# Kernel tuning notes

Hardware: AMD Instinct MI355X
Metric: run time of the kernel (lower is better)

The kernel has to match this reference:

```python
import jax, jax.numpy as jnp
import numpy as np

N = 50000      # nodes
E = 1600000    # edges
IN_DIM = 128
HID = 32
OUT = 32
HEADS = 4
NEG_SLOPE = 0.2  # DGL GATConv default leaky_relu slope


def setup_inputs() -> dict:
    key = jax.random.key(0)
    ks = jax.random.split(key, 16)
    h = jax.random.normal(ks[0], (N, IN_DIM), dtype=jnp.float32)
    src = jax.random.randint(ks[1], (E,), 0, N, dtype=jnp.int32)
    dst = jax.random.randint(ks[2], (E,), 0, N, dtype=jnp.int32)
    s = 0.1
    # layer 1: in_dim -> (HEADS, HID)
    W1 = jax.random.normal(ks[3], (IN_DIM, HEADS * HID), dtype=jnp.float32) * s
    al1 = jax.random.normal(ks[4], (HEADS, HID), dtype=jnp.float32) * s
    ar1 = jax.random.normal(ks[5], (HEADS, HID), dtype=jnp.float32) * s
    b1 = jnp.zeros((HEADS * HID,), dtype=jnp.float32)
    # layer 2: HEADS*HID -> (HEADS, HID)
    W2 = jax.random.normal(ks[6], (HEADS * HID, HEADS * HID), dtype=jnp.float32) * s
    al2 = jax.random.normal(ks[7], (HEADS, HID), dtype=jnp.float32) * s
    ar2 = jax.random.normal(ks[8], (HEADS, HID), dtype=jnp.float32) * s
    b2 = jnp.zeros((HEADS * HID,), dtype=jnp.float32)
    # layer 3: HEADS*HID -> (HEADS, OUT)
    W3 = jax.random.normal(ks[9], (HEADS * HID, HEADS * OUT), dtype=jnp.float32) * s
    al3 = jax.random.normal(ks[10], (HEADS, OUT), dtype=jnp.float32) * s
    ar3 = jax.random.normal(ks[11], (HEADS, OUT), dtype=jnp.float32) * s
    b3 = jnp.zeros((HEADS * OUT,), dtype=jnp.float32)
    return {"h": h, "src": src, "dst": dst,
            "W1": W1, "al1": al1, "ar1": ar1, "b1": b1,
            "W2": W2, "al2": al2, "ar2": ar2, "b2": b2,
            "W3": W3, "al3": al3, "ar3": ar3, "b3": b3}


def gat_layer(h, W, al, ar, b, src, dst):
    """DGL-style GATConv. h:[N,F] -> [N,H,D]."""
    H, D = al.shape
    ft = (h @ W).reshape(-1, H, D)                      # [N,H,D]
    el = jnp.einsum('nhd,hd->nh', ft, al)               # [N,H]
    er = jnp.einsum('nhd,hd->nh', ft, ar)               # [N,H]
    e = jax.nn.leaky_relu(el[src] + er[dst], NEG_SLOPE)  # [E,H]
    # edge softmax grouped by destination node
    m = jax.ops.segment_max(e, dst, num_segments=N)     # [N,H]
    ex = jnp.exp(e - m[dst])
    z = jax.ops.segment_sum(ex, dst, num_segments=N)    # [N,H]
    a = ex / z[dst]                                     # [E,H]
    msg = ft[src] * a[:, :, None]                       # [E,H,D]
    rst = jax.ops.segment_sum(msg, dst, num_segments=N)  # [N,H,D]
    return rst + b.reshape(1, H, D)


def reference(h, src, dst, W1, al1, ar1, b1, W2, al2, ar2, b2, W3, al3, ar3, b3):
    x = gat_layer(h, W1, al1, ar1, b1, src, dst).reshape(N, -1)  # flatten(1)
    x = jax.nn.elu(x)  # dropout is identity at eval
    x = gat_layer(x, W2, al2, ar2, b2, src, dst).reshape(N, -1)
    x = jax.nn.elu(x)
    x = gat_layer(x, W3, al3, ar3, b3, src, dst).mean(axis=1)    # [N,OUT]
    return x
```

## Files before the change

### kernel.cpp

```cpp
#include <hip/hip_runtime.h>
#include <hip/hip_fp16.h>

#define NEG_SLOPE 0.2f
#define LOG2E 1.44269504088896340736f
#define C1   2048
#define BKT  196
#define BSTR 9216

typedef _Float16 half8 __attribute__((ext_vector_type(8)));

__device__ __forceinline__ unsigned int encf(float f) {
    unsigned int u = __float_as_uint(f);
    return (u & 0x80000000u) ? ~u : (u | 0x80000000u);
}
__device__ __forceinline__ float decf(unsigned int u) {
    return (u & 0x80000000u) ? __uint_as_float(u & 0x7fffffffu)
                             : __uint_as_float(~u);
}

__global__ __launch_bounds__(256) void gemm128(const float* __restrict__ X,
    const float* __restrict__ W, const float* __restrict__ al,
    const float* __restrict__ ar, __half* __restrict__ C16,
    float* __restrict__ el, float* __restrict__ er,
    unsigned int* __restrict__ maxbuf, int M)
{
    __shared__ float Xs[32][68];
    __shared__ float Ws[32][128];
    __shared__ unsigned int lmax[8];
    const int t    = threadIdx.x;
    const int row0 = blockIdx.x * 64;
    const int rg   = t >> 5;
    const int cg   = t & 31;
    float acc[8][4];
#pragma unroll
    for (int i = 0; i < 8; ++i) { acc[i][0]=0.f; acc[i][1]=0.f; acc[i][2]=0.f; acc[i][3]=0.f; }
    if (t < 8) lmax[t] = 0;

    for (int kc = 0; kc < 4; ++kc) {
        const int k0 = kc * 32;
        {
            const int lr = t >> 2;
            const int lk = (t & 3) * 8;
            int gr = row0 + lr; if (gr >= M) gr = M - 1;
            const float4* s4 = (const float4*)&X[(size_t)gr * 128 + k0 + lk];
            float4 a = s4[0], b = s4[1];
            Xs[lk+0][lr]=a.x; Xs[lk+1][lr]=a.y; Xs[lk+2][lr]=a.z; Xs[lk+3][lr]=a.w;
            Xs[lk+4][lr]=b.x; Xs[lk+5][lr]=b.y; Xs[lk+6][lr]=b.z; Xs[lk+7][lr]=b.w;
        }
        {
            const int lk = t >> 3;
            const int lc = (t & 7) * 16;
            const float4* s4 = (const float4*)&W[(size_t)(k0 + lk) * 128 + lc];
            float4* dd = (float4*)&Ws[lk][lc];
            dd[0]=s4[0]; dd[1]=s4[1]; dd[2]=s4[2]; dd[3]=s4[3];
        }
        __syncthreads();
#pragma unroll
        for (int k = 0; k < 32; ++k) {
            float4 wv = *(const float4*)&Ws[k][cg * 4];
            float4 x0 = *(const float4*)&Xs[k][rg * 8];
            float4 x1 = *(const float4*)&Xs[k][rg * 8 + 4];
            float xr[8] = {x0.x,x0.y,x0.z,x0.w,x1.x,x1.y,x1.z,x1.w};
#pragma unroll
            for (int i = 0; i < 8; ++i) {
                acc[i][0] += xr[i] * wv.x;
                acc[i][1] += xr[i] * wv.y;
                acc[i][2] += xr[i] * wv.z;
                acc[i][3] += xr[i] * wv.w;
            }
        }
        __syncthreads();
    }
#pragma unroll
    for (int i = 0; i < 8; ++i) {
        int gr = row0 + rg * 8 + i;
        if (gr < M) {
            __half2 h0 = __floats2half2_rn(acc[i][0], acc[i][1]);
            __half2 h1 = __floats2half2_rn(acc[i][2], acc[i][3]);
            uint2 pv;
            pv.x = __builtin_bit_cast(unsigned int, h0);
            pv.y = __builtin_bit_cast(unsigned int, h1);
            *(uint2*)&C16[(size_t)gr * 128 + cg * 4] = pv;
        }
    }
    {
        float4 alv = *(const float4*)&al[cg * 4];
        float4 arv = *(const float4*)&ar[cg * 4];
        alv.x *= LOG2E; alv.y *= LOG2E; alv.z *= LOG2E; alv.w *= LOG2E;
        arv.x *= LOG2E; arv.y *= LOG2E; arv.z *= LOG2E; arv.w *= LOG2E;
        float pl[8], pr[8];
#pragma unroll
        for (int i = 0; i < 8; ++i) {
            pl[i] = acc[i][0]*alv.x + acc[i][1]*alv.y + acc[i][2]*alv.z + acc[i][3]*alv.w;
            pr[i] = acc[i][0]*arv.x + acc[i][1]*arv.y + acc[i][2]*arv.z + acc[i][3]*arv.w;
        }
#pragma unroll
        for (int off = 1; off < 8; off <<= 1) {
#pragma unroll
            for (int i = 0; i < 8; ++i) {
                pl[i] += __shfl_xor(pl[i], off);
                pr[i] += __shfl_xor(pr[i], off);
            }
        }
        if ((cg & 7) == 0) {
            const int head = cg >> 3;
            float plm = pl[0], prm = pr[0];
#pragma unroll
            for (int i = 1; i < 8; ++i) { plm = fmaxf(plm, pl[i]); prm = fmaxf(prm, pr[i]); }
            atomicMax(&lmax[head], encf(plm));
            atomicMax(&lmax[4 + head], encf(prm));
#pragma unroll
            for (int i = 0; i < 8; ++i) {
                int gr = row0 + rg * 8 + i;
                if (gr < M) {
                    el[(size_t)gr * 4 + head] = pl[i];
                    er[(size_t)gr * 4 + head] = pr[i];
                }
            }
        }
        __syncthreads();
        if (t < 8) atomicMax(&maxbuf[t], lmax[t]);
    }
}

__global__ __launch_bounds__(256) void p1_bucket(const int* __restrict__ src,
    const int* __restrict__ dst, unsigned int* __restrict__ tmp,
    unsigned int* __restrict__ bcnt, int E_)
{
    __shared__ unsigned int hist[256];
    __shared__ unsigned int sc[256];
    __shared__ unsigned int ebase[256];
    __shared__ unsigned int gbase[256];
    __shared__ unsigned int buf[C1];
    const int t  = threadIdx.x;
    const int e0 = blockIdx.x * C1;
    hist[t] = 0;
    __syncthreads();
    int  s_[8], d_[8];
    bool v_[8];
#pragma unroll
    for (int k = 0; k < 2; ++k) {
        int idx = e0 + k * 1024 + t * 4;
        if (idx + 3 < E_) {
            int4 sv = *(const int4*)&src[idx];
            int4 dv = *(const int4*)&dst[idx];
            s_[k*4+0]=sv.x; s_[k*4+1]=sv.y; s_[k*4+2]=sv.z; s_[k*4+3]=sv.w;
            d_[k*4+0]=dv.x; d_[k*4+1]=dv.y; d_[k*4+2]=dv.z; d_[k*4+3]=dv.w;
            v_[k*4+0]=true; v_[k*4+1]=true; v_[k*4+2]=true; v_[k*4+3]=true;
        } else {
            for (int j = 0; j < 4; ++j) {
                int e = idx + j;
                v_[k*4+j] = e < E_;
                s_[k*4+j] = v_[k*4+j] ? src[e] : 0;
                d_[k*4+j] = v_[k*4+j] ? dst[e] : 0;
            }
        }
    }
#pragma unroll
    for (int j = 0; j < 8; ++j) if (v_[j]) atomicAdd(&hist[d_[j] >> 8], 1u);
    __syncthreads();
    const unsigned int cnt_t = hist[t];
    sc[t] = cnt_t;
    __syncthreads();
    for (int off = 1; off < 256; off <<= 1) {
        unsigned int v = (t >= off) ? sc[t - off] : 0;
        __syncthreads();
        sc[t] += v;
        __syncthreads();
    }
    const unsigned int excl = sc[t] - cnt_t;
    ebase[t] = excl;
    gbase[t] = (t < BKT && cnt_t > 0) ? atomicAdd(&bcnt[t], cnt_t) : 0u;
    hist[t] = excl;
    __syncthreads();
#pragma unroll
    for (int j = 0; j < 8; ++j) {
        if (v_[j]) {
            int b = d_[j] >> 8;
            unsigned int pos = atomicAdd(&hist[b], 1u);
            buf[pos] = ((unsigned int)s_[j] << 8) | (unsigned int)(d_[j] & 255);
        }
    }
    __syncthreads();
    const int total = min(C1, E_ - e0);
    for (int i = t; i < total; i += 256) {
        int lo = 0, hi = 255;
        while (lo < hi) { int mid = (lo + hi) >> 1; if (sc[mid] > (unsigned int)i) hi = mid; else lo = mid + 1; }
        unsigned int off = gbase[lo] + ((unsigned int)i - ebase[lo]);
        if (off < BSTR) tmp[(size_t)lo * BSTR + off] = buf[i];
    }
}

__global__ __launch_bounds__(256) void scanB(const unsigned int* __restrict__ bcnt,
    unsigned int* __restrict__ bbase, unsigned int* __restrict__ maxinit, int E_)
{
    __shared__ unsigned int sc[256];
    const int t = threadIdx.x;
    const unsigned int v = (t < BKT) ? bcnt[t] : 0;
    sc[t] = v;
    __syncthreads();
    for (int off = 1; off < 256; off <<= 1) {
        unsigned int u = (t >= off) ? sc[t - off] : 0;
        __syncthreads();
        sc[t] += u;
        __syncthreads();
    }
    if (t < BKT) bbase[t] = sc[t] - v;
    if (t == BKT) bbase[t] = (unsigned int)E_;
    if (t < 24) maxinit[t] = 0;
}

__global__ __launch_bounds__(256) void p2_scatter(const unsigned int* __restrict__ tmp,
    const unsigned int* __restrict__ bcnt, const unsigned int* __restrict__ bbase,
    int* __restrict__ rowptr, int* __restrict__ esrc_s, int Nn)
{
    __shared__ unsigned int hist[256], sc[256], cur[256];
    __shared__ unsigned int ent[BSTR];
    const int t = threadIdx.x;
    const int b = blockIdx.x;
    const unsigned int cnt  = min(bcnt[b], (unsigned int)BSTR);
    const unsigned int base = bbase[b];
    hist[t] = 0;
    __syncthreads();
    for (unsigned int i = t; i < cnt; i += 256) {
        unsigned int e = tmp[(size_t)b * BSTR + i];
        ent[i] = e;
        atomicAdd(&hist[e & 255u], 1u);
    }
    __syncthreads();
    const unsigned int c_t = hist[t];
    sc[t] = c_t;
    __syncthreads();
    for (int off = 1; off < 256; off <<= 1) {
        unsigned int u = (t >= off) ? sc[t - off] : 0;
        __syncthreads();
        sc[t] += u;
        __syncthreads();
    }
    const unsigned int excl = sc[t] - c_t;
    cur[t] = base + excl;
    const int n = (b << 8) + t;
    if (n <= Nn) rowptr[n] = (int)(base + excl);
    __syncthreads();
    for (unsigned int i = t; i < cnt; i += 256) {
        unsigned int e = ent[i];
        unsigned int p = atomicAdd(&cur[e & 255u], 1u);
        esrc_s[p] = (int)(e >> 8);
    }
}

template <int MODE>
__global__ __launch_bounds__(256) void attn_agg(
    const __half* __restrict__ ft, const float* __restrict__ el,
    const float* __restrict__ er, const int* __restrict__ rowptr,
    const int* __restrict__ esrc, const float* __restrict__ bias,
    const unsigned int* __restrict__ mbuf, float* __restrict__ out, int Nn)
{
    const int t = threadIdx.x;
    const int l = t & 63;
    const int n = blockIdx.x * 4 + (t >> 6);
    if (n >= Nn) return;
    const int g    = l >> 4;
    const int q    = l & 15;
    const int head = q >> 2;

    const int start = rowptr[n];
    const int end   = rowptr[n + 1];
    const bool any  = end > start;

    const float er_h = er[(size_t)n * 4 + head];
    const float msum = decf(mbuf[head]) + decf(mbuf[4 + head]);
    const float mh   = msum > 0.f ? msum : NEG_SLOPE * msum;

    const char* __restrict__ ftb = (const char*)ft;
    const char* __restrict__ elb = (const char*)el;
    const unsigned qo = (unsigned)q << 4;
    const unsigned ho = (unsigned)head << 2;

    float acc[8];
#pragma unroll
    for (int j = 0; j < 8; ++j) acc[j] = 0.f;
    float z = 0.f;

    const int c0   = start & ~3;
    const int last = end - 1;
    const int span = end - start;

    int  sA = 0, sB = 0, sC = 0;
    uint4 fA = make_uint4(0,0,0,0), fB;
    float eA = 0.f, eB;

    if (any) {
        int e0i = min(max(c0 + g, start), last);
        int e1i = min(max(c0 + 4 + g, start), last);
        sA = esrc[e0i];
        sB = esrc[e1i];
        fA = *(const uint4*)(ftb + ((unsigned)sA << 8) + qo);
        eA = *(const float*)(elb + ((unsigned)sA << 4) + ho);
    }

#pragma unroll 2
    for (int c = c0; c < end; c += 4) {
        sC = esrc[min(c + 8 + g, last)];
        fB = *(const uint4*)(ftb + ((unsigned)sB << 8) + qo);
        eB = *(const float*)(elb + ((unsigned)sB << 4) + ho);
        {
            const int e = c + g;
            float x = eA + er_h;
            x = fmaxf(x, NEG_SLOPE * x);
            float ex = __builtin_amdgcn_exp2f(x - mh);
            ex = ((unsigned)(e - start) < (unsigned)span) ? ex : 0.f;
            z += ex;
            const half8 hv = __builtin_bit_cast(half8, fA);
            acc[0] += (float)hv[0] * ex;
            acc[1] += (float)hv[1] * ex;
            acc[2] += (float)hv[2] * ex;
            acc[3] += (float)hv[3] * ex;
            acc[4] += (float)hv[4] * ex;
            acc[5] += (float)hv[5] * ex;
            acc[6] += (float)hv[6] * ex;
            acc[7] += (float)hv[7] * ex;
        }
        sA = sB; sB = sC; fA = fB; eA = eB;
    }

#pragma unroll
    for (int j = 0; j < 8; ++j) {
        acc[j] += __shfl_xor(acc[j], 16);
        acc[j] += __shfl_xor(acc[j], 32);
    }
    z += __shfl_xor(z, 16);
    z += __shfl_xor(z, 32);

    const float inv = any ? 1.f / z : 0.f;

    if (MODE == 0) {
        if (l < 32) {
            float r0, r1, r2, r3;
            if (l < 16) { r0 = acc[0]; r1 = acc[1]; r2 = acc[2]; r3 = acc[3]; }
            else        { r0 = acc[4]; r1 = acc[5]; r2 = acc[6]; r3 = acc[7]; }
            const int f0 = 8 * q + 4 * (l >> 4);
            const float4 b4 = *(const float4*)&bias[f0];
            float vx = r0 * inv + b4.x;
            float vy = r1 * inv + b4.y;
            float vz = r2 * inv + b4.z;
            float vw = r3 * inv + b4.w;
            vx = vx > 0.f ? vx : __expf(vx) - 1.f;
            vy = vy > 0.f ? vy : __expf(vy) - 1.f;
            vz = vz > 0.f ? vz : __expf(vz) - 1.f;
            vw = vw > 0.f ? vw : __expf(vw) - 1.f;
            *(float4*)&out[(size_t)n * 128 + f0] = make_float4(vx, vy, vz, vw);
        }
    } else {
        float v[8];
        const float4 ba = *(const float4*)&bias[8 * q];
        const float4 bb = *(const float4*)&bias[8 * q + 4];
        v[0] = acc[0] * inv + ba.x; v[1] = acc[1] * inv + ba.y;
        v[2] = acc[2] * inv + ba.z; v[3] = acc[3] * inv + ba.w;
        v[4] = acc[4] * inv + bb.x; v[5] = acc[5] * inv + bb.y;
        v[6] = acc[6] * inv + bb.z; v[7] = acc[7] * inv + bb.w;
#pragma unroll
        for (int j = 0; j < 8; ++j) {
            v[j] += __shfl_xor(v[j], 4);
            v[j] += __shfl_xor(v[j], 8);
        }
        if (l < 4) {
            *(float4*)&out[(size_t)n * 32 + 8 * q] =
                make_float4(0.25f * v[0], 0.25f * v[1], 0.25f * v[2], 0.25f * v[3]);
            *(float4*)&out[(size_t)n * 32 + 8 * q + 4] =
                make_float4(0.25f * v[4], 0.25f * v[5], 0.25f * v[6], 0.25f * v[7]);
        }
    }
}

extern "C" void kernel_launch(void* const* d_in, const int* in_sizes, int n_in,
                              void* d_out, int out_size, void* d_ws, size_t ws_size,
                              hipStream_t stream)
{
    const float* h   = (const float*)d_in[0];
    const int*   src = (const int*)d_in[1];
    const int*   dst = (const int*)d_in[2];
    const float* W1  = (const float*)d_in[3];
    const float* al1 = (const float*)d_in[4];
    const float* ar1 = (const float*)d_in[5];
    const float* b1  = (const float*)d_in[6];
    const float* W2  = (const float*)d_in[7];
    const float* al2 = (const float*)d_in[8];
    const float* ar2 = (const float*)d_in[9];
    const float* b2  = (const float*)d_in[10];
    const float* W3  = (const float*)d_in[11];
    const float* al3 = (const float*)d_in[12];
    const float* ar3 = (const float*)d_in[13];
    const float* b3  = (const float*)d_in[14];

    const int N = in_sizes[0] / 128;
    const int E = in_sizes[1];

    char* p = (char*)d_ws;
    auto alloc = [&](size_t bytes) {
        void* r = (void*)p;
        p += (bytes + 255) & ~(size_t)255;
        return r;
    };
    __half* ft    = (__half*)alloc((size_t)N * 128 * 4);
    float* xA     = (float*)alloc((size_t)N * 128 * 4);
    float* elbuf  = (float*)alloc((size_t)N * 4 * 4);
    float* erbuf  = (float*)alloc((size_t)N * 4 * 4);
    int*   rowptr = (int*)alloc((size_t)(N + 1) * 4);
    int*   esrc_s = (int*)alloc((size_t)E * 4);
    unsigned int* bcnt   = (unsigned int*)alloc((size_t)BKT * 4);
    unsigned int* bbase  = (unsigned int*)alloc((size_t)(BKT + 1) * 4);
    unsigned int* maxbuf = (unsigned int*)alloc(24 * 4);

    unsigned int* tmp = (unsigned int*)ft;

    const int NG4 = (N + 3) / 4;
    const int MG  = (N + 63) / 64;
    const int G1  = (E + C1 - 1) / C1;

    hipMemsetAsync(bcnt, 0, (size_t)BKT * 4, stream);
    p1_bucket<<<G1, 256, 0, stream>>>(src, dst, tmp, bcnt, E);
    scanB<<<1, 256, 0, stream>>>(bcnt, bbase, maxbuf, E);
    p2_scatter<<<BKT, 256, 0, stream>>>(tmp, bcnt, bbase, rowptr, esrc_s, N);

    gemm128<<<MG, 256, 0, stream>>>(h, W1, al1, ar1, ft, elbuf, erbuf, maxbuf, N);
    attn_agg<0><<<NG4, 256, 0, stream>>>(ft, elbuf, erbuf, rowptr, esrc_s, b1, maxbuf, xA, N);

    gemm128<<<MG, 256, 0, stream>>>(xA, W2, al2, ar2, ft, elbuf, erbuf, maxbuf + 8, N);
    attn_agg<0><<<NG4, 256, 0, stream>>>(ft, elbuf, erbuf, rowptr, esrc_s, b2, maxbuf + 8, xA, N);

    gemm128<<<MG, 256, 0, stream>>>(xA, W3, al3, ar3, ft, elbuf, erbuf, maxbuf + 16, N);
    attn_agg<1><<<NG4, 256, 0, stream>>>(ft, elbuf, erbuf, rowptr, esrc_s, b3, maxbuf + 16,
                                         (float*)d_out, N);
}
```

Measured before the change: 398.0 us.

## Replace FP32 FMA GEMM with FP16 MFMA GEMM using pre-transposed half weights

Swaps the per-layer scalar FP32 GEMM for one built on MFMA 16x16x32 f16 instructions. Inputs are converted to half in swizzled LDS, and a new wprep kernel transposes and converts all three weight matrices to half once. The attention logit projections and per-head max are computed from the MFMA accumulators, and the fp16 output is staged through LDS so global stores are coalesced. This cuts GEMM compute time at the cost of rounding inputs and weights to fp16, and adds one small extra launch.

```diff
diff --git a/kernel.cpp b/kernel.cpp
--- a/kernel.cpp
+++ b/kernel.cpp
@@ -8,6 +8,7 @@
 #define BSTR 9216
 
 typedef _Float16 half8 __attribute__((ext_vector_type(8)));
+typedef float    f32x4 __attribute__((ext_vector_type(4)));
 
 __device__ __forceinline__ unsigned int encf(float f) {
     unsigned int u = __float_as_uint(f);
@@ -18,109 +19,175 @@
                              : __uint_as_float(~u);
 }
 
-__global__ __launch_bounds__(256) void gemm128(const float* __restrict__ X,
-    const float* __restrict__ W, const float* __restrict__ al,
+__global__ __launch_bounds__(256) void wprep(const float* __restrict__ W1,
+    const float* __restrict__ W2, const float* __restrict__ W3,
+    __half* __restrict__ Wt)
+{
+    __shared__ float tile[32][33];
+    const int b = blockIdx.x;
+    const float* W = (b < 16) ? W1 : (b < 32) ? W2 : W3;
+    __half* out = Wt + (size_t)(b >> 4) * (128 * 128);
+    const int tb = b & 15;
+    const int k0 = (tb >> 2) * 32;
+    const int c0 = (tb & 3) * 32;
+    const int t = threadIdx.x;
+    const int tx = t & 31, ty = t >> 5;
+#pragma unroll
+    for (int p = 0; p < 4; ++p)
+        tile[p * 8 + ty][tx] = W[(size_t)(k0 + p * 8 + ty) * 128 + c0 + tx];
+    __syncthreads();
+#pragma unroll
+    for (int p = 0; p < 4; ++p) {
+        const int c = c0 + p * 8 + ty;
+        out[(size_t)c * 128 + k0 + tx] = __float2half(tile[tx][p * 8 + ty]);
+    }
+}
+
+__global__ __launch_bounds__(256) void gemm_mfma(const float* __restrict__ X,
+    const __half* __restrict__ Wt, const float* __restrict__ al,
     const float* __restrict__ ar, __half* __restrict__ C16,
     float* __restrict__ el, float* __restrict__ er,
     unsigned int* __restrict__ maxbuf, int M)
 {
-    __shared__ float Xs[32][68];
-    __shared__ float Ws[32][128];
+    __shared__ __align__(16) char Xs[64 * 256];
+    __shared__ __align__(16) char Ws[128 * 256];
     __shared__ unsigned int lmax[8];
-    const int t    = threadIdx.x;
+    const int t = threadIdx.x;
+    const int l = t & 63;
+    const int w = t >> 6;
     const int row0 = blockIdx.x * 64;
-    const int rg   = t >> 5;
-    const int cg   = t & 31;
-    float acc[8][4];
-#pragma unroll
-    for (int i = 0; i < 8; ++i) { acc[i][0]=0.f; acc[i][1]=0.f; acc[i][2]=0.f; acc[i][3]=0.f; }
     if (t < 8) lmax[t] = 0;
 
-    for (int kc = 0; kc < 4; ++kc) {
-        const int k0 = kc * 32;
-        {
-            const int lr = t >> 2;
-            const int lk = (t & 3) * 8;
-            int gr = row0 + lr; if (gr >= M) gr = M - 1;
-            const float4* s4 = (const float4*)&X[(size_t)gr * 128 + k0 + lk];
-            float4 a = s4[0], b = s4[1];
-            Xs[lk+0][lr]=a.x; Xs[lk+1][lr]=a.y; Xs[lk+2][lr]=a.z; Xs[lk+3][lr]=a.w;
-            Xs[lk+4][lr]=b.x; Xs[lk+5][lr]=b.y; Xs[lk+6][lr]=b.z; Xs[lk+7][lr]=b.w;
-        }
-        {
-            const int lk = t >> 3;
-            const int lc = (t & 7) * 16;
-            const float4* s4 = (const float4*)&W[(size_t)(k0 + lk) * 128 + lc];
-            float4* dd = (float4*)&Ws[lk][lc];
-            dd[0]=s4[0]; dd[1]=s4[1]; dd[2]=s4[2]; dd[3]=s4[3];
-        }
-        __syncthreads();
-#pragma unroll
-        for (int k = 0; k < 32; ++k) {
-            float4 wv = *(const float4*)&Ws[k][cg * 4];
-            float4 x0 = *(const float4*)&Xs[k][rg * 8];
-            float4 x1 = *(const float4*)&Xs[k][rg * 8 + 4];
-            float xr[8] = {x0.x,x0.y,x0.z,x0.w,x1.x,x1.y,x1.z,x1.w};
-#pragma unroll
-            for (int i = 0; i < 8; ++i) {
-                acc[i][0] += xr[i] * wv.x;
-                acc[i][1] += xr[i] * wv.y;
-                acc[i][2] += xr[i] * wv.z;
-                acc[i][3] += xr[i] * wv.w;
+    {
+        const int r = t >> 2;
+        int gr = row0 + r; if (gr >= M) gr = M - 1;
+        const float4* s4 = (const float4*)&X[(size_t)gr * 128 + (t & 3) * 32];
+        const unsigned swz = ((unsigned)(r & 7)) << 4;
+        char* base = Xs + r * 256;
+#pragma unroll
+        for (int u = 0; u < 4; ++u) {
+            float4 a = s4[2 * u], b = s4[2 * u + 1];
+            half8 hv;
+            hv[0] = (_Float16)a.x; hv[1] = (_Float16)a.y;
+            hv[2] = (_Float16)a.z; hv[3] = (_Float16)a.w;
+            hv[4] = (_Float16)b.x; hv[5] = (_Float16)b.y;
+            hv[6] = (_Float16)b.z; hv[7] = (_Float16)b.w;
+            *(half8*)(base + (((t & 3) * 64 + u * 16) ^ swz)) = hv;
+        }
+    }
+    {
+        const int c = t >> 1;
+        const char* src = (const char*)Wt + (size_t)c * 256 + (t & 1) * 128;
+        const unsigned swz = ((unsigned)(c & 7)) << 4;
+        char* base = Ws + c * 256;
+#pragma unroll
+        for (int u = 0; u < 8; ++u) {
+            uint4 v = *(const uint4*)(src + u * 16);
+            *(uint4*)(base + (((t & 1) * 128 + u * 16) ^ swz)) = v;
+        }
+    }
+    __syncthreads();
+
+    const int wr = w * 16;
+    const int rA = l & 15;
+    const int kq = l >> 4;
+
+    half8 af[4];
+    {
+        const int row = wr + rA;
+        const unsigned swz = ((unsigned)(row & 7)) << 4;
+        const char* base = Xs + row * 256;
+#pragma unroll
+        for (int kk = 0; kk < 4; ++kk)
+            af[kk] = *(const half8*)(base + (((unsigned)(kk * 64 + kq * 16)) ^ swz));
+    }
+    f32x4 acc[8];
+#pragma unroll
+    for (int ct = 0; ct < 8; ++ct) { acc[ct][0]=0.f; acc[ct][1]=0.f; acc[ct][2]=0.f; acc[ct][3]=0.f; }
+#pragma unroll
+    for (int ct = 0; ct < 8; ++ct) {
+        const int c = ct * 16 + rA;
+        const unsigned swz = ((unsigned)(c & 7)) << 4;
+        const char* base = Ws + c * 256;
+#pragma unroll
+        for (int kk = 0; kk < 4; ++kk) {
+            half8 bf = *(const half8*)(base + (((unsigned)(kk * 64 + kq * 16)) ^ swz));
+            acc[ct] = __builtin_amdgcn_mfma_f32_16x16x32_f16(af[kk], bf, acc[ct], 0, 0, 0);
+        }
+    }
+
+    float pl[4][4], pr[4][4];
+#pragma unroll
+    for (int h = 0; h < 4; ++h)
+#pragma unroll
+        for (int r = 0; r < 4; ++r) { pl[h][r] = 0.f; pr[h][r] = 0.f; }
+#pragma unroll
+    for (int ct = 0; ct < 8; ++ct) {
+        const int col = ct * 16 + rA;
+        const float av = al[col] * LOG2E;
+        const float rv = ar[col] * LOG2E;
+        const int h = ct >> 1;
+#pragma unroll
+        for (int r = 0; r < 4; ++r) {
+            pl[h][r] += acc[ct][r] * av;
+            pr[h][r] += acc[ct][r] * rv;
+        }
+    }
+#pragma unroll
+    for (int off = 1; off < 16; off <<= 1) {
+#pragma unroll
+        for (int h = 0; h < 4; ++h)
+#pragma unroll
+            for (int r = 0; r < 4; ++r) {
+                pl[h][r] += __shfl_xor(pl[h][r], off);
+                pr[h][r] += __shfl_xor(pr[h][r], off);
             }
-        }
-        __syncthreads();
-    }
-#pragma unroll
-    for (int i = 0; i < 8; ++i) {
-        int gr = row0 + rg * 8 + i;
-        if (gr < M) {
-            __half2 h0 = __floats2half2_rn(acc[i][0], acc[i][1]);
-            __half2 h1 = __floats2half2_rn(acc[i][2], acc[i][3]);
-            uint2 pv;
-            pv.x = __builtin_bit_cast(unsigned int, h0);
-            pv.y = __builtin_bit_cast(unsigned int, h1);
-            *(uint2*)&C16[(size_t)gr * 128 + cg * 4] = pv;
-        }
-    }
+    }
+    if (rA == 0) {
+#pragma unroll
+        for (int r = 0; r < 4; ++r) {
+            const int gr = row0 + wr + kq * 4 + r;
+            if (gr < M) {
+                *(float4*)&el[(size_t)gr * 4] =
+                    make_float4(pl[0][r], pl[1][r], pl[2][r], pl[3][r]);
+                *(float4*)&er[(size_t)gr * 4] =
+                    make_float4(pr[0][r], pr[1][r], pr[2][r], pr[3][r]);
+            }
+        }
+#pragma unroll
+        for (int h = 0; h < 4; ++h) {
+            float ml = fmaxf(fmaxf(pl[h][0], pl[h][1]), fmaxf(pl[h][2], pl[h][3]));
+            float mr = fmaxf(fmaxf(pr[h][0], pr[h][1]), fmaxf(pr[h][2], pr[h][3]));
+            atomicMax(&lmax[h], encf(ml));
+            atomicMax(&lmax[4 + h], encf(mr));
+        }
+    }
+
     {
-        float4 alv = *(const float4*)&al[cg * 4];
-        float4 arv = *(const float4*)&ar[cg * 4];
-        alv.x *= LOG2E; alv.y *= LOG2E; alv.z *= LOG2E; alv.w *= LOG2E;
-        arv.x *= LOG2E; arv.y *= LOG2E; arv.z *= LOG2E; arv.w *= LOG2E;
-        float pl[8], pr[8];
-#pragma unroll
-        for (int i = 0; i < 8; ++i) {
-            pl[i] = acc[i][0]*alv.x + acc[i][1]*alv.y + acc[i][2]*alv.z + acc[i][3]*alv.w;
-            pr[i] = acc[i][0]*arv.x + acc[i][1]*arv.y + acc[i][2]*arv.z + acc[i][3]*arv.w;
-        }
-#pragma unroll
-        for (int off = 1; off < 8; off <<= 1) {
-#pragma unroll
-            for (int i = 0; i < 8; ++i) {
-                pl[i] += __shfl_xor(pl[i], off);
-                pr[i] += __shfl_xor(pr[i], off);
+        char* slice = Xs + wr * 256;
+#pragma unroll
+        for (int ct = 0; ct < 8; ++ct) {
+            const int colb = (ct * 16 + rA) * 2;
+#pragma unroll
+            for (int r = 0; r < 4; ++r) {
+                const int rowL = kq * 4 + r;
+                const unsigned swz = ((unsigned)(rowL & 7)) << 4;
+                *(__half*)(slice + rowL * 256 + ((unsigned)colb ^ swz)) =
+                    __float2half(acc[ct][r]);
             }
         }
-        if ((cg & 7) == 0) {
-            const int head = cg >> 3;
-            float plm = pl[0], prm = pr[0];
-#pragma unroll
-            for (int i = 1; i < 8; ++i) { plm = fmaxf(plm, pl[i]); prm = fmaxf(prm, pr[i]); }
-            atomicMax(&lmax[head], encf(plm));
-            atomicMax(&lmax[4 + head], encf(prm));
-#pragma unroll
-            for (int i = 0; i < 8; ++i) {
-                int gr = row0 + rg * 8 + i;
-                if (gr < M) {
-                    el[(size_t)gr * 4 + head] = pl[i];
-                    er[(size_t)gr * 4 + head] = pr[i];
-                }
-            }
-        }
-        __syncthreads();
-        if (t < 8) atomicMax(&maxbuf[t], lmax[t]);
-    }
+        const int rowL = l >> 2;
+        const unsigned swz = ((unsigned)(rowL & 7)) << 4;
+        const int gr = row0 + wr + rowL;
+#pragma unroll
+        for (int u = 0; u < 4; ++u) {
+            const unsigned bo = (unsigned)((l & 3) * 64 + u * 16);
+            uint4 v = *(const uint4*)(slice + rowL * 256 + (bo ^ swz));
+            if (gr < M) *(uint4*)&C16[(size_t)gr * 128 + bo / 2] = v;
+        }
+    }
+    __syncthreads();
+    if (t < 8) atomicMax(&maxbuf[t], lmax[t]);
 }
 
 __global__ __launch_bounds__(256) void p1_bucket(const int* __restrict__ src,
@@ -411,6 +478,7 @@
     unsigned int* bcnt   = (unsigned int*)alloc((size_t)BKT * 4);
     unsigned int* bbase  = (unsigned int*)alloc((size_t)(BKT + 1) * 4);
     unsigned int* maxbuf = (unsigned int*)alloc(24 * 4);
+    __half* Wt    = (__half*)alloc((size_t)3 * 128 * 128 * 2);
 
     unsigned int* tmp = (unsigned int*)ft;
 
@@ -419,17 +487,18 @@
     const int G1  = (E + C1 - 1) / C1;
 
     hipMemsetAsync(bcnt, 0, (size_t)BKT * 4, stream);
+    wprep<<<48, 256, 0, stream>>>(W1, W2, W3, Wt);
     p1_bucket<<<G1, 256, 0, stream>>>(src, dst, tmp, bcnt, E);
     scanB<<<1, 256, 0, stream>>>(bcnt, bbase, maxbuf, E);
     p2_scatter<<<BKT, 256, 0, stream>>>(tmp, bcnt, bbase, rowptr, esrc_s, N);
 
-    gemm128<<<MG, 256, 0, stream>>>(h, W1, al1, ar1, ft, elbuf, erbuf, maxbuf, N);
+    gemm_mfma<<<MG, 256, 0, stream>>>(h, Wt, al1, ar1, ft, elbuf, erbuf, maxbuf, N);
     attn_agg<0><<<NG4, 256, 0, stream>>>(ft, elbuf, erbuf, rowptr, esrc_s, b1, maxbuf, xA, N);
 
-    gemm128<<<MG, 256, 0, stream>>>(xA, W2, al2, ar2, ft, elbuf, erbuf, maxbuf + 8, N);
+    gemm_mfma<<<MG, 256, 0, stream>>>(xA, Wt + 128 * 128, al2, ar2, ft, elbuf, erbuf, maxbuf + 8, N);
     attn_agg<0><<<NG4, 256, 0, stream>>>(ft, elbuf, erbuf, rowptr, esrc_s, b2, maxbuf + 8, xA, N);
 
-    gemm128<<<MG, 256, 0, stream>>>(xA, W3, al3, ar3, ft, elbuf, erbuf, maxbuf + 16, N);
+    gemm_mfma<<<MG, 256, 0, stream>>>(xA, Wt + 2 * 128 * 128, al3, ar3, ft, elbuf, erbuf, maxbuf + 16, N);
     attn_agg<1><<<NG4, 256, 0, stream>>>(ft, elbuf, erbuf, rowptr, esrc_s, b3, maxbuf + 16,
                                          (float*)d_out, N);
 }
```

New measurement: 391.0 us. No clear change (-1.7%).
